# Kernel optimization log

Hardware: AMD Instinct MI355X
Metric: run time of the kernel (lower is better)

## Reference

```python
import jax, jax.numpy as jnp
import numpy as np

B, N, E, D_IN, D_OUT = 8, 8192, 131072, 128, 128
LN_EPS = 1e-5

def setup_inputs() -> dict:
    key = jax.random.key(0)
    k1, k2, k3, k4 = jax.random.split(key, 4)
    node_features = jax.random.normal(k1, (B, N, D_IN), dtype=jnp.float32)
    edge_index = jax.random.randint(k2, (B, 2, E), 0, N, dtype=jnp.int64)
    node_mask = jnp.ones((B, N), dtype=jnp.float32)
    # Linear params (torch Linear: y = x @ W.T + b)
    W = jax.random.normal(k3, (D_OUT, D_IN), dtype=jnp.float32) / np.sqrt(D_IN)
    b = jax.random.normal(k4, (D_OUT,), dtype=jnp.float32) * 0.01
    # LayerNorm params
    gamma = jnp.ones((D_OUT,), dtype=jnp.float32)
    beta = jnp.zeros((D_OUT,), dtype=jnp.float32)
    return {"node_features": node_features, "edge_index": edge_index,
            "node_mask": node_mask, "W": W, "b": b, "gamma": gamma, "beta": beta}

def reference(node_features, edge_index, node_mask, W, b, gamma, beta):
    max_nodes = node_features.shape[1]
    h = jnp.einsum('bni,oi->bno', node_features, W) + b  # [B,N,D_OUT]
    def agg_one(hb, eb):
        # gather source features then scatter-add into targets
        return jax.ops.segment_sum(hb[eb[0]], eb[1], num_segments=max_nodes)
    aggregated = jax.vmap(agg_one)(h, edge_index)  # [B,N,D_OUT]
    h = h + aggregated / jnp.sqrt(jnp.float32(max_nodes))
    # dropout is identity in eval mode
    mu = jnp.mean(h, axis=-1, keepdims=True)
    var = jnp.mean((h - mu) ** 2, axis=-1, keepdims=True)
    h = (h - mu) * jax.lax.rsqrt(var + LN_EPS) * gamma + beta
    h = jax.nn.relu(h)
    return h * node_mask[..., None]
```

## Files before the change

kernel.cpp:

```cpp
#include <hip/hip_runtime.h>

#define B_ 8
#define N_ 8192
#define E_ 131072
#define D_ 128
#define M_ (B_ * N_)
#define SLOTS 64
#define NCH 32
#define CHE (E_ / NCH)
constexpr float INV_SQRT_N = 0.011048543456039806f;
constexpr float LN_EPS_C = 1e-5f;

typedef __attribute__((ext_vector_type(8))) short bf16x8;
typedef __attribute__((ext_vector_type(4))) float f32x4;
typedef __attribute__((ext_vector_type(4))) float f32x4v;
typedef __attribute__((ext_vector_type(4))) unsigned u32x4;

static __device__ __forceinline__ unsigned short f2bf(float f) {
  unsigned u = __float_as_uint(f);
  u += 0x7fffu + ((u >> 16) & 1u);
  return (unsigned short)(u >> 16);
}
static __device__ __forceinline__ float bflo(unsigned u) {
  return __uint_as_float(u << 16);
}
static __device__ __forceinline__ float bfhi(unsigned u) {
  return __uint_as_float(u & 0xffff0000u);
}
static __device__ __forceinline__ bf16x8 cvt8v(const f32x4v a, const f32x4v b) {
  bf16x8 r;
  r[0] = (short)f2bf(a.x); r[1] = (short)f2bf(a.y);
  r[2] = (short)f2bf(a.z); r[3] = (short)f2bf(a.w);
  r[4] = (short)f2bf(b.x); r[5] = (short)f2bf(b.y);
  r[6] = (short)f2bf(b.z); r[7] = (short)f2bf(b.w);
  return r;
}

__global__ __launch_bounds__(256, 2) void gemm_count_kernel(
    const float* __restrict__ X, const float* __restrict__ W,
    const float* __restrict__ bias, const int* __restrict__ eidx,
    unsigned short* __restrict__ histc, unsigned short* __restrict__ hb) {
  __shared__ unsigned hist[N_];
  if (blockIdx.x < 256) {
    const int wave = threadIdx.x >> 6;
    const int lane = threadIdx.x & 63;
    const int m16 = lane & 15;
    const int q = lane >> 4;
    const int hf = wave & 1;
    const int ng = wave >> 1;

    bf16x8 wf[4][4];
#pragma unroll
    for (int kt4 = 0; kt4 < 4; ++kt4) {
#pragma unroll
      for (int tt = 0; tt < 4; ++tt) {
        const float* wr = W + (size_t)(hf * 64 + tt * 16 + m16) * D_ +
                          kt4 * 32 + q * 8;
        wf[kt4][tt] = cvt8v(*(const f32x4v*)wr, *(const f32x4v*)(wr + 4));
      }
    }

    const int bi = blockIdx.x;
    const int nbase0 = (bi & 7) * N_ + (bi >> 3) * 256 + ng * 128;
#pragma unroll 2
    for (int s = 0; s < 8; ++s) {
      const int nbase = nbase0 + s * 16;
      const float* xrow = X + (size_t)(nbase + m16) * D_;

      f32x4 acc[4];
#pragma unroll
      for (int tt = 0; tt < 4; ++tt) acc[tt] = (f32x4){0.f, 0.f, 0.f, 0.f};

#pragma unroll
      for (int kt4 = 0; kt4 < 4; ++kt4) {
        const f32x4v xa = __builtin_nontemporal_load(
            (const f32x4v*)(xrow + kt4 * 32 + q * 8));
        const f32x4v xb = __builtin_nontemporal_load(
            (const f32x4v*)(xrow + kt4 * 32 + q * 8 + 4));
        const bf16x8 xf = cvt8v(xa, xb);
#pragma unroll
        for (int tt = 0; tt < 4; ++tt) {
          acc[tt] = __builtin_amdgcn_mfma_f32_16x16x32_bf16(wf[kt4][tt], xf,
                                                            acc[tt], 0, 0, 0);
        }
      }

      const size_t orow = (size_t)(nbase + m16) * D_;
#pragma unroll
      for (int tt = 0; tt < 4; ++tt) {
        const int f0 = hf * 64 + tt * 16 + q * 4;
        const float4 b4 = *(const float4*)&bias[f0];
        uint2 uu;
        uu.x = (unsigned)f2bf(acc[tt][0] + b4.x) |
               ((unsigned)f2bf(acc[tt][1] + b4.y) << 16);
        uu.y = (unsigned)f2bf(acc[tt][2] + b4.z) |
               ((unsigned)f2bf(acc[tt][3] + b4.w) << 16);
        *(uint2*)(hb + orow + f0) = uu;
      }
    }
  } else {
    const int f = blockIdx.x - 256;
    const int b = f & 7;
    const int c = f >> 3;
    const int t = threadIdx.x;

#pragma unroll
    for (int i = 0; i < N_ / 256; ++i) hist[t + i * 256] = 0u;
    __syncthreads();

    const int* __restrict__ tgtp = eidx + b * 2 * E_ + E_ + c * CHE;
#pragma unroll
    for (int k = 0; k < 4; ++k) {
      const int4 tv = *(const int4*)(tgtp + t * 16 + k * 4);
      atomicAdd(&hist[tv.x], 1u);
      atomicAdd(&hist[tv.y], 1u);
      atomicAdd(&hist[tv.z], 1u);
      atomicAdd(&hist[tv.w], 1u);
    }
    __syncthreads();

    unsigned* dst = (unsigned*)(histc + ((size_t)b * NCH + c) * N_);
#pragma unroll
    for (int i = 0; i < N_ / 512; ++i) {
      const int j = t + i * 256;
      const unsigned lo = hist[2 * j];
      const unsigned hi = hist[2 * j + 1];
      dst[j] = (lo & 0xffffu) | (hi << 16);
    }
  }
}

__global__ __launch_bounds__(256, 8) void prefix_kernel(
    unsigned short* __restrict__ histc, int* __restrict__ cnt) {
  const int b = blockIdx.x & 7;
  const int nb = blockIdx.x >> 3;
  const int n = nb * 256 + threadIdx.x;
  unsigned short* base = histc + (size_t)b * NCH * N_ + n;
  unsigned short v[NCH];
#pragma unroll
  for (int c = 0; c < NCH; ++c) v[c] = base[(size_t)c * N_];
  unsigned run = 0;
#pragma unroll
  for (int c = 0; c < NCH; ++c) {
    const unsigned x = v[c];
    base[(size_t)c * N_] = (unsigned short)run;
    run += x;
  }
  cnt[b * N_ + n] = (int)run;
}

__global__ __launch_bounds__(256, 2) void place_kernel(
    const int* __restrict__ eidx, const unsigned short* __restrict__ histc,
    unsigned short* __restrict__ bucket) {
  __shared__ unsigned hist[N_];
  const int b = blockIdx.x & 7;
  const int c = blockIdx.x >> 3;
  const int t = threadIdx.x;

#pragma unroll
  for (int i = 0; i < N_ / 256; ++i) hist[t + i * 256] = 0u;
  __syncthreads();

  const int* __restrict__ srcp = eidx + b * 2 * E_ + c * CHE;
  const int* __restrict__ tgtp = srcp + E_;
  const unsigned short* __restrict__ basep = histc + ((size_t)b * NCH + c) * N_;
  unsigned short* __restrict__ bkt = bucket + (size_t)b * N_ * SLOTS;

#pragma unroll
  for (int k = 0; k < 4; ++k) {
    const int4 tv = *(const int4*)(tgtp + t * 16 + k * 4);
    const int4 sv = *(const int4*)(srcp + t * 16 + k * 4);
    const unsigned b0 = basep[tv.x];
    const unsigned b1 = basep[tv.y];
    const unsigned b2 = basep[tv.z];
    const unsigned b3 = basep[tv.w];
    const unsigned p0 = atomicAdd(&hist[tv.x], 1u) + b0;
    const unsigned p1 = atomicAdd(&hist[tv.y], 1u) + b1;
    const unsigned p2 = atomicAdd(&hist[tv.z], 1u) + b2;
    const unsigned p3 = atomicAdd(&hist[tv.w], 1u) + b3;
    if (p0 < SLOTS) bkt[(size_t)tv.x * SLOTS + p0] = (unsigned short)sv.x;
    if (p1 < SLOTS) bkt[(size_t)tv.y * SLOTS + p1] = (unsigned short)sv.y;
    if (p2 < SLOTS) bkt[(size_t)tv.z * SLOTS + p2] = (unsigned short)sv.z;
    if (p3 < SLOTS) bkt[(size_t)tv.w * SLOTS + p3] = (unsigned short)sv.w;
  }
}

__global__ __launch_bounds__(256, 8) void gather_finalize_kernel(
    const unsigned short* __restrict__ hb, const unsigned short* __restrict__ bucket,
    const int* __restrict__ cnt, const float* __restrict__ mask,
    const float* __restrict__ gamma, const float* __restrict__ beta,
    float* __restrict__ out) {
  const int bid = blockIdx.x;
  const int batch = bid & 7;
  const int wave = threadIdx.x >> 6;
  const int lane = threadIdx.x & 63;
  const int g = lane >> 4;
  const int c = lane & 15;
  const int r = (bid >> 3) * 16 + wave * 4 + g;
  const int row = batch * N_ + r;

  const u32x4* hub4 = (const u32x4*)hb + (size_t)batch * N_ * 16;

  const int deg = min(cnt[row], SLOTS);
  const uint2 su = *(const uint2*)&bucket[(size_t)row * SLOTS + c * 4];
  const u32x4 ur = hub4[r * 16 + c];
  const float m = mask[row];

  float a[8];
#pragma unroll
  for (int k = 0; k < 8; ++k) a[k] = 0.f;

  int jb = 0;
  for (; jb + 8 <= deg; jb += 8) {
    const int L = jb >> 2;
    const unsigned w0 = (unsigned)__shfl((int)su.x, L, 16);
    const unsigned w1 = (unsigned)__shfl((int)su.y, L, 16);
    const unsigned w2 = (unsigned)__shfl((int)su.x, L + 1, 16);
    const unsigned w3 = (unsigned)__shfl((int)su.y, L + 1, 16);
    const int idx[8] = {(int)(w0 & 0xffff), (int)(w0 >> 16),
                        (int)(w1 & 0xffff), (int)(w1 >> 16),
                        (int)(w2 & 0xffff), (int)(w2 >> 16),
                        (int)(w3 & 0xffff), (int)(w3 >> 16)};
    u32x4 v[8];
#pragma unroll
    for (int i = 0; i < 8; ++i) v[i] = hub4[idx[i] * 16 + c];
#pragma unroll
    for (int i = 0; i < 8; ++i) {
      a[0] += bflo(v[i].x); a[1] += bfhi(v[i].x);
      a[2] += bflo(v[i].y); a[3] += bfhi(v[i].y);
      a[4] += bflo(v[i].z); a[5] += bfhi(v[i].z);
      a[6] += bflo(v[i].w); a[7] += bfhi(v[i].w);
    }
  }
  for (; jb < deg; ++jb) {
    const int L = jb >> 2;
    const unsigned w = ((jb >> 1) & 1) ? (unsigned)__shfl((int)su.y, L, 16)
                                       : (unsigned)__shfl((int)su.x, L, 16);
    const int idx = (jb & 1) ? (int)(w >> 16) : (int)(w & 0xffff);
    const u32x4 v = hub4[idx * 16 + c];
    a[0] += bflo(v.x); a[1] += bfhi(v.x);
    a[2] += bflo(v.y); a[3] += bfhi(v.y);
    a[4] += bflo(v.z); a[5] += bfhi(v.z);
    a[6] += bflo(v.w); a[7] += bfhi(v.w);
  }

  float x[8];
  x[0] = bflo(ur.x) + a[0] * INV_SQRT_N;
  x[1] = bfhi(ur.x) + a[1] * INV_SQRT_N;
  x[2] = bflo(ur.y) + a[2] * INV_SQRT_N;
  x[3] = bfhi(ur.y) + a[3] * INV_SQRT_N;
  x[4] = bflo(ur.z) + a[4] * INV_SQRT_N;
  x[5] = bfhi(ur.z) + a[5] * INV_SQRT_N;
  x[6] = bflo(ur.w) + a[6] * INV_SQRT_N;
  x[7] = bfhi(ur.w) + a[7] * INV_SQRT_N;

  float s0 = 0.f, ss = 0.f;
#pragma unroll
  for (int k = 0; k < 8; ++k) {
    s0 += x[k];
    ss += x[k] * x[k];
  }
#pragma unroll
  for (int o = 8; o >= 1; o >>= 1) {
    s0 += __shfl_xor(s0, o, 16);
    ss += __shfl_xor(ss, o, 16);
  }
  const float mu = s0 * (1.f / 128.f);
  float var = ss * (1.f / 128.f) - mu * mu;
  var = var < 0.f ? 0.f : var;
  const float rstd = rsqrtf(var + LN_EPS_C);

  const f32x4v g0 = *((const f32x4v*)gamma + c * 2);
  const f32x4v g1 = *((const f32x4v*)gamma + c * 2 + 1);
  const f32x4v b0 = *((const f32x4v*)beta + c * 2);
  const f32x4v b1 = *((const f32x4v*)beta + c * 2 + 1);

  f32x4v o0, o1;
  o0.x = (x[0] - mu) * rstd * g0.x + b0.x;
  o0.y = (x[1] - mu) * rstd * g0.y + b0.y;
  o0.z = (x[2] - mu) * rstd * g0.z + b0.z;
  o0.w = (x[3] - mu) * rstd * g0.w + b0.w;
  o1.x = (x[4] - mu) * rstd * g1.x + b1.x;
  o1.y = (x[5] - mu) * rstd * g1.y + b1.y;
  o1.z = (x[6] - mu) * rstd * g1.z + b1.z;
  o1.w = (x[7] - mu) * rstd * g1.w + b1.w;
  o0.x = (o0.x > 0.f ? o0.x : 0.f) * m;
  o0.y = (o0.y > 0.f ? o0.y : 0.f) * m;
  o0.z = (o0.z > 0.f ? o0.z : 0.f) * m;
  o0.w = (o0.w > 0.f ? o0.w : 0.f) * m;
  o1.x = (o1.x > 0.f ? o1.x : 0.f) * m;
  o1.y = (o1.y > 0.f ? o1.y : 0.f) * m;
  o1.z = (o1.z > 0.f ? o1.z : 0.f) * m;
  o1.w = (o1.w > 0.f ? o1.w : 0.f) * m;

  f32x4v* op = (f32x4v*)out + (size_t)row * 32 + c * 2;
  __builtin_nontemporal_store(o0, op);
  __builtin_nontemporal_store(o1, op + 1);
}

extern "C" void kernel_launch(void* const* d_in, const int* in_sizes, int n_in,
                              void* d_out, int out_size, void* d_ws,
                              size_t ws_size, hipStream_t stream) {
  const float* X = (const float*)d_in[0];
  const int* eidx = (const int*)d_in[1];
  const float* mask = (const float*)d_in[2];
  const float* W = (const float*)d_in[3];
  const float* bias = (const float*)d_in[4];
  const float* gamma = (const float*)d_in[5];
  const float* beta = (const float*)d_in[6];
  float* out = (float*)d_out;

  unsigned short* hb = (unsigned short*)d_ws;
  unsigned short* bucket = hb + (size_t)M_ * D_;
  int* cnt = (int*)(bucket + (size_t)M_ * SLOTS);
  unsigned short* histc = (unsigned short*)out;

  gemm_count_kernel<<<512, 256, 0, stream>>>(X, W, bias, eidx, histc, hb);
  prefix_kernel<<<256, 256, 0, stream>>>(histc, cnt);
  place_kernel<<<256, 256, 0, stream>>>(eidx, histc, bucket);
  gather_finalize_kernel<<<M_ / 16, 256, 0, stream>>>(hb, bucket, cnt, mask,
                                                      gamma, beta, out);
}
```

Measured before the change: 147.0 us.

## Record per-edge ranks during counting so placement skips LDS histogram

The count pass now saves each edge's local atomic rank into a 16-bit rank buffer. The place kernel reads that rank and no longer rebuilds a shared-memory histogram with atomics. This lets it drop the 32KB LDS array and run four times as many small blocks. The gather loop also folds its scalar tail into the 8-wide loop, masking invalid lanes with predicated loads. The cost is an extra rank-buffer write and read in global memory.

After: 153.6 us. 4.5% more time.

```diff
diff --git a/kernel.cpp b/kernel.cpp
--- a/kernel.cpp
+++ b/kernel.cpp
@@ -39,7 +39,8 @@
 __global__ __launch_bounds__(256, 2) void gemm_count_kernel(
     const float* __restrict__ X, const float* __restrict__ W,
     const float* __restrict__ bias, const int* __restrict__ eidx,
-    unsigned short* __restrict__ histc, unsigned short* __restrict__ hb) {
+    unsigned short* __restrict__ histc, unsigned short* __restrict__ rankb,
+    unsigned short* __restrict__ hb) {
   __shared__ unsigned hist[N_];
   if (blockIdx.x < 256) {
     const int wave = threadIdx.x >> 6;
@@ -109,13 +110,18 @@
     __syncthreads();
 
     const int* __restrict__ tgtp = eidx + b * 2 * E_ + E_ + c * CHE;
+    unsigned short* __restrict__ rnk = rankb + (size_t)b * E_ + c * CHE;
 #pragma unroll
     for (int k = 0; k < 4; ++k) {
       const int4 tv = *(const int4*)(tgtp + t * 16 + k * 4);
-      atomicAdd(&hist[tv.x], 1u);
-      atomicAdd(&hist[tv.y], 1u);
-      atomicAdd(&hist[tv.z], 1u);
-      atomicAdd(&hist[tv.w], 1u);
+      const unsigned r0 = atomicAdd(&hist[tv.x], 1u);
+      const unsigned r1 = atomicAdd(&hist[tv.y], 1u);
+      const unsigned r2 = atomicAdd(&hist[tv.z], 1u);
+      const unsigned r3 = atomicAdd(&hist[tv.w], 1u);
+      uint2 rr;
+      rr.x = (r0 & 0xffffu) | (r1 << 16);
+      rr.y = (r2 & 0xffffu) | (r3 << 16);
+      *(uint2*)(rnk + t * 16 + k * 4) = rr;
     }
     __syncthreads();
 
@@ -149,40 +155,31 @@
   cnt[b * N_ + n] = (int)run;
 }
 
-__global__ __launch_bounds__(256, 2) void place_kernel(
+__global__ __launch_bounds__(256, 8) void place_kernel(
     const int* __restrict__ eidx, const unsigned short* __restrict__ histc,
+    const unsigned short* __restrict__ rankb,
     unsigned short* __restrict__ bucket) {
-  __shared__ unsigned hist[N_];
   const int b = blockIdx.x & 7;
-  const int c = blockIdx.x >> 3;
+  const int pos = blockIdx.x >> 3;
+  const int c = pos >> 2;
   const int t = threadIdx.x;
-
-#pragma unroll
-  for (int i = 0; i < N_ / 256; ++i) hist[t + i * 256] = 0u;
-  __syncthreads();
-
-  const int* __restrict__ srcp = eidx + b * 2 * E_ + c * CHE;
-  const int* __restrict__ tgtp = srcp + E_;
+  const int e0 = pos * 1024 + t * 4;
+
+  const int* __restrict__ srcp = eidx + b * 2 * E_;
+  const int4 tv = *(const int4*)(srcp + E_ + e0);
+  const int4 sv = *(const int4*)(srcp + e0);
+  const uint2 rr = *(const uint2*)(rankb + (size_t)b * E_ + e0);
   const unsigned short* __restrict__ basep = histc + ((size_t)b * NCH + c) * N_;
   unsigned short* __restrict__ bkt = bucket + (size_t)b * N_ * SLOTS;
 
-#pragma unroll
-  for (int k = 0; k < 4; ++k) {
-    const int4 tv = *(const int4*)(tgtp + t * 16 + k * 4);
-    const int4 sv = *(const int4*)(srcp + t * 16 + k * 4);
-    const unsigned b0 = basep[tv.x];
-    const unsigned b1 = basep[tv.y];
-    const unsigned b2 = basep[tv.z];
-    const unsigned b3 = basep[tv.w];
-    const unsigned p0 = atomicAdd(&hist[tv.x], 1u) + b0;
-    const unsigned p1 = atomicAdd(&hist[tv.y], 1u) + b1;
-    const unsigned p2 = atomicAdd(&hist[tv.z], 1u) + b2;
-    const unsigned p3 = atomicAdd(&hist[tv.w], 1u) + b3;
-    if (p0 < SLOTS) bkt[(size_t)tv.x * SLOTS + p0] = (unsigned short)sv.x;
-    if (p1 < SLOTS) bkt[(size_t)tv.y * SLOTS + p1] = (unsigned short)sv.y;
-    if (p2 < SLOTS) bkt[(size_t)tv.z * SLOTS + p2] = (unsigned short)sv.z;
-    if (p3 < SLOTS) bkt[(size_t)tv.w * SLOTS + p3] = (unsigned short)sv.w;
-  }
+  const unsigned p0 = (unsigned)basep[tv.x] + (rr.x & 0xffffu);
+  const unsigned p1 = (unsigned)basep[tv.y] + (rr.x >> 16);
+  const unsigned p2 = (unsigned)basep[tv.z] + (rr.y & 0xffffu);
+  const unsigned p3 = (unsigned)basep[tv.w] + (rr.y >> 16);
+  if (p0 < SLOTS) bkt[(size_t)tv.x * SLOTS + p0] = (unsigned short)sv.x;
+  if (p1 < SLOTS) bkt[(size_t)tv.y * SLOTS + p1] = (unsigned short)sv.y;
+  if (p2 < SLOTS) bkt[(size_t)tv.z * SLOTS + p2] = (unsigned short)sv.z;
+  if (p3 < SLOTS) bkt[(size_t)tv.w * SLOTS + p3] = (unsigned short)sv.w;
 }
 
 __global__ __launch_bounds__(256, 8) void gather_finalize_kernel(
@@ -210,8 +207,7 @@
 #pragma unroll
   for (int k = 0; k < 8; ++k) a[k] = 0.f;
 
-  int jb = 0;
-  for (; jb + 8 <= deg; jb += 8) {
+  for (int jb = 0; jb < deg; jb += 8) {
     const int L = jb >> 2;
     const unsigned w0 = (unsigned)__shfl((int)su.x, L, 16);
     const unsigned w1 = (unsigned)__shfl((int)su.y, L, 16);
@@ -223,7 +219,13 @@
                         (int)(w3 & 0xffff), (int)(w3 >> 16)};
     u32x4 v[8];
 #pragma unroll
-    for (int i = 0; i < 8; ++i) v[i] = hub4[idx[i] * 16 + c];
+    for (int i = 0; i < 8; ++i) {
+      const bool val = (jb + i) < deg;
+      const int id = val ? idx[i] : 0;
+      u32x4 tv = hub4[id * 16 + c];
+      if (!val) tv = (u32x4){0u, 0u, 0u, 0u};
+      v[i] = tv;
+    }
 #pragma unroll
     for (int i = 0; i < 8; ++i) {
       a[0] += bflo(v[i].x); a[1] += bfhi(v[i].x);
@@ -231,17 +233,6 @@
       a[4] += bflo(v[i].z); a[5] += bfhi(v[i].z);
       a[6] += bflo(v[i].w); a[7] += bfhi(v[i].w);
     }
-  }
-  for (; jb < deg; ++jb) {
-    const int L = jb >> 2;
-    const unsigned w = ((jb >> 1) & 1) ? (unsigned)__shfl((int)su.y, L, 16)
-                                       : (unsigned)__shfl((int)su.x, L, 16);
-    const int idx = (jb & 1) ? (int)(w >> 16) : (int)(w & 0xffff);
-    const u32x4 v = hub4[idx * 16 + c];
-    a[0] += bflo(v.x); a[1] += bfhi(v.x);
-    a[2] += bflo(v.y); a[3] += bfhi(v.y);
-    a[4] += bflo(v.z); a[5] += bfhi(v.z);
-    a[6] += bflo(v.w); a[7] += bfhi(v.w);
   }
 
   float x[8];
@@ -313,11 +304,13 @@
   unsigned short* hb = (unsigned short*)d_ws;
   unsigned short* bucket = hb + (size_t)M_ * D_;
   int* cnt = (int*)(bucket + (size_t)M_ * SLOTS);
+  unsigned short* rankb = (unsigned short*)(cnt + M_);
   unsigned short* histc = (unsigned short*)out;
 
-  gemm_count_kernel<<<512, 256, 0, stream>>>(X, W, bias, eidx, histc, hb);
+  gemm_count_kernel<<<512, 256, 0, stream>>>(X, W, bias, eidx, histc, rankb,
+                                             hb);
   prefix_kernel<<<256, 256, 0, stream>>>(histc, cnt);
-  place_kernel<<<256, 256, 0, stream>>>(eidx, histc, bucket);
+  place_kernel<<<1024, 256, 0, stream>>>(eidx, histc, rankb, bucket);
   gather_finalize_kernel<<<M_ / 16, 256, 0, stream>>>(hb, bucket, cnt, mask,
                                                       gamma, beta, out);
 }
```
